# Performance work log

Hardware: AMD Instinct MI355X
Metric: run time of the kernel (lower is better)

## Reference

```python
import jax, jax.numpy as jnp
import numpy as np

DIM = 512
MAXP = 100
N_SAMPLED = MAXP - 2  # partitions 0 (whole) and 1 (singletons) handled analytically
KMAX = 6              # sampled partitions have 2..6 parts


def _make_part_masks(dim, n_sampled, kmax, seed=0):
    rng = np.random.default_rng(seed)
    masks = np.zeros((n_sampled, kmax, dim), dtype=bool)
    for p in range(n_sampled):
        n_parts = rng.integers(2, kmax + 1)
        assign = rng.integers(0, n_parts, size=dim)
        for k in range(n_parts):
            masks[p, k] = assign == k
    return masks


def setup_inputs() -> dict:
    key = jax.random.key(0)
    ks = jax.random.split(key, 10)
    B, S, D = 8, 4096, DIM
    x = jax.random.normal(ks[0], (B, S, D), dtype=jnp.float32)
    entropy_scales = jnp.ones((D,), dtype=jnp.float32)
    integration_weights = jnp.ones((MAXP,), dtype=jnp.float32)
    W1 = jax.random.normal(ks[1], (32, 1), dtype=jnp.float32) * 0.5
    b1 = jax.random.normal(ks[2], (32,), dtype=jnp.float32) * 0.1
    W2 = jax.random.normal(ks[3], (16, 32), dtype=jnp.float32) * 0.2
    b2 = jax.random.normal(ks[4], (16,), dtype=jnp.float32) * 0.1
    W3 = jax.random.normal(ks[5], (1, 16), dtype=jnp.float32) * 0.3
    b3 = jax.random.normal(ks[6], (1,), dtype=jnp.float32) * 0.1
    part_masks = jnp.asarray(_make_part_masks(D, N_SAMPLED, KMAX))  # [P,K,D] bool
    return {"x": x, "entropy_scales": entropy_scales,
            "integration_weights": integration_weights,
            "W1": W1, "b1": b1, "W2": W2, "b2": b2, "W3": W3, "b3": b3,
            "part_masks": part_masks}


def _phi(x, entropy_scales, integration_weights, W1, b1, W2, b2, W3, b3, part_masks):
    B, S, D = x.shape
    # ---- full-flatten entropy (per batch), H(softmax(x.reshape(B,-1))) ----
    lp = jax.nn.log_softmax(x.reshape(B, -1), axis=-1)
    H_full = -jnp.sum(jnp.exp(lp) * lp, axis=-1)                     # [B]
    h_full_scaled = H_full * entropy_scales.mean()                   # [B]
    h_whole = H_full.mean()                                          # partition idx 0

    # ---- singleton partition (idx 1): softmax over seq per (b,d) ----
    lps = jax.nn.log_softmax(x, axis=1)                              # [B,S,D]
    H_sd = -jnp.sum(jnp.exp(lps) * lps, axis=1)                      # [B,D]
    h_single = H_sd.mean(axis=0).sum()

    # ---- sampled partitions via masks: per part, softmax over (seq x part dims) ----
    xmax_d = x.max(axis=1)                                           # [B,D]
    ex = jnp.exp(x - xmax_d[:, None, :])                             # [B,S,D]
    e_d = ex.sum(axis=1)                                             # [B,D] sum exp(x - xmax_d)
    t_d = (ex * x).sum(axis=1)                                       # [B,D] sum exp(.)*x
    valid = part_masks.any(axis=-1)                                  # [P,K]
    neg = jnp.finfo(x.dtype).min
    gmax = jnp.max(jnp.where(part_masks[None], xmax_d[:, None, None, :], neg), axis=-1)  # [B,P,K]
    gmax = jnp.where(valid[None], gmax, 0.0)
    shift = jnp.exp(xmax_d[:, None, None, :] - gmax[..., None])      # [B,P,K,D] <= 1
    mf = part_masks.astype(x.dtype)
    Z = jnp.einsum('pkd,bd,bpkd->bpk', mf, e_d, shift)               # group partition fn
    T = jnp.einsum('pkd,bd,bpkd->bpk', mf, t_d, shift)
    Zs = jnp.where(valid[None], Z, 1.0)
    H_pk = gmax + jnp.log(Zs) - T / Zs                               # group entropy [B,P,K]
    H_pk = jnp.where(valid[None], H_pk, 0.0)
    h_sampled = H_pk.mean(axis=0).sum(axis=-1)                       # [P] sum of part entropies

    h_parts = jnp.concatenate([jnp.stack([h_whole, h_single]), h_sampled])   # [100]
    weighted = h_parts * jax.nn.sigmoid(integration_weights[: h_parts.shape[0]])
    min_part = weighted.min()

    raw_phi = h_full_scaled.mean() - min_part
    z = jnp.clip(raw_phi / 10.0, 0.0, 1.0)[None]                     # [1]
    h = jax.nn.relu(z @ W1.T + b1)
    h = jax.nn.relu(h @ W2.T + b2)
    conf = jax.nn.sigmoid(h @ W3.T + b3).squeeze(-1)                 # scalar
    return conf


def reference(x, entropy_scales, integration_weights, W1, b1, W2, b2, W3, b3, part_masks):
    return _phi(x, entropy_scales, integration_weights, W1, b1, W2, b2, W3, b3, part_masks)
```

## Files before the change

### kernel.cpp

```cpp
#include <hip/hip_runtime.h>
#include <math.h>

constexpr int Bv = 8;
constexpr int Sv = 4096;
constexpr int Dv = 512;
constexpr int NCv = 64;
constexpr int SCv = Sv / NCv;
constexpr int Pv = 98;
constexpr int Kv = 6;
constexpr int MAXPv = 100;

constexpr size_t OFF_MPART = 0;
constexpr size_t OFF_ZPART = OFF_MPART + (size_t)Bv * NCv * Dv;
constexpr size_t OFF_TPART = OFF_ZPART + (size_t)Bv * NCv * Dv;
constexpr size_t OFF_XMAX  = OFF_TPART + (size_t)Bv * NCv * Dv;
constexpr size_t OFF_ED    = OFF_XMAX + (size_t)Bv * Dv;
constexpr size_t OFF_TD    = OFF_ED   + (size_t)Bv * Dv;
constexpr size_t OFF_HFULL = OFF_TD   + (size_t)Bv * Dv;
constexpr size_t OFF_HSD   = OFF_HFULL + Bv;
constexpr size_t OFF_HBP   = OFF_HSD + Bv;
constexpr size_t OFF_ASSIGN = OFF_HBP + (size_t)Bv * Pv;

__device__ __forceinline__ float warpSum(float v) {
    for (int o = 32; o > 0; o >>= 1) v += __shfl_xor(v, o);
    return v;
}
__device__ __forceinline__ float warpMax(float v) {
    for (int o = 32; o > 0; o >>= 1) v = fmaxf(v, __shfl_xor(v, o));
    return v;
}
__device__ __forceinline__ float blockSum512(float v, float* red) {
    float s = warpSum(v);
    int lane = threadIdx.x & 63, w = threadIdx.x >> 6;
    __syncthreads();
    if (lane == 0) red[w] = s;
    __syncthreads();
    return red[0] + red[1] + red[2] + red[3] + red[4] + red[5] + red[6] + red[7];
}
__device__ __forceinline__ float blockMax512(float v, float* red) {
    float s = warpMax(v);
    int lane = threadIdx.x & 63, w = threadIdx.x >> 6;
    __syncthreads();
    if (lane == 0) red[w] = s;
    __syncthreads();
    float m = red[0];
    for (int i = 1; i < 8; i++) m = fmaxf(m, red[i]);
    return m;
}

__device__ __forceinline__ unsigned int encf(float f) {
    unsigned int u = __float_as_uint(f);
    return (u & 0x80000000u) ? ~u : (u | 0x80000000u);
}
__device__ __forceinline__ float decf(unsigned int u) {
    return (u & 0x80000000u) ? __uint_as_float(u ^ 0x80000000u) : __uint_as_float(~u);
}

#define UPD(v, m, z, t)                                        \
    {                                                          \
        float vv = (v);                                        \
        if (vv > m) {                                          \
            float r = __expf(m - vv);                          \
            z = z * r + 1.0f;                                  \
            t = t * r + vv;                                    \
            m = vv;                                            \
        } else {                                               \
            float e_ = __expf(vv - m);                         \
            z += e_;                                           \
            t += e_ * vv;                                      \
        }                                                      \
    }

__device__ __forceinline__ void mergeStats(float& m, float& z, float& t,
                                           float mb, float zb, float tb) {
    float nm = fmaxf(m, mb);
    float ra = __expf(m - nm);
    float rb = __expf(mb - nm);
    z = z * ra + zb * rb;
    t = t * ra + tb * rb;
    m = nm;
}

__global__ __launch_bounds__(512) void k_assign(const void* __restrict__ masks,
                                                float* __restrict__ ws) {
    int p = blockIdx.x;
    int d = threadIdx.x;
    __shared__ int f;
    if (d == 0) f = 0;
    __syncthreads();
    const unsigned int* mw = (const unsigned int*)masks;
    if (mw[d] > 1u || mw[d + 512] > 1u) atomicOr(&f, 1);
    __syncthreads();
    int is_u8 = f;

    unsigned char a = 255;
    if (is_u8) {
        const unsigned char* mb = (const unsigned char*)masks;
        for (int k = 0; k < Kv; k++) {
            if (mb[((size_t)p * Kv + k) * Dv + d]) { a = (unsigned char)k; break; }
        }
    } else {
        const int* mi = (const int*)masks;
        for (int k = 0; k < Kv; k++) {
            if (mi[((size_t)p * Kv + k) * Dv + d]) { a = (unsigned char)k; break; }
        }
    }
    ((unsigned char*)(ws + OFF_ASSIGN))[(size_t)p * Dv + d] = a;
}

__global__ __launch_bounds__(256) void k1_partial(const float* __restrict__ x,
                                                  float* __restrict__ ws) {
    int c = blockIdx.x;
    int b = blockIdx.y;
    int tid = threadIdx.x;
    int dg = tid & 127;
    int sl = tid >> 7;

    const float4* xv = (const float4*)x;
    float m0 = -INFINITY, m1 = -INFINITY, m2 = -INFINITY, m3 = -INFINITY;
    float z0 = 0.f, z1 = 0.f, z2 = 0.f, z3 = 0.f;
    float t0 = 0.f, t1 = 0.f, t2 = 0.f, t3 = 0.f;

    int sbase = c * SCv + sl;
    for (int i = 0; i < SCv / 2; i++) {
        int s = sbase + 2 * i;
        float4 v = xv[((size_t)b * Sv + s) * 128 + dg];
        UPD(v.x, m0, z0, t0);
        UPD(v.y, m1, z1, t1);
        UPD(v.z, m2, z2, t2);
        UPD(v.w, m3, z3, t3);
    }

    __shared__ float smm[128 * 4], smz[128 * 4], smt[128 * 4];
    if (sl == 1) {
        smm[dg * 4 + 0] = m0; smm[dg * 4 + 1] = m1; smm[dg * 4 + 2] = m2; smm[dg * 4 + 3] = m3;
        smz[dg * 4 + 0] = z0; smz[dg * 4 + 1] = z1; smz[dg * 4 + 2] = z2; smz[dg * 4 + 3] = z3;
        smt[dg * 4 + 0] = t0; smt[dg * 4 + 1] = t1; smt[dg * 4 + 2] = t2; smt[dg * 4 + 3] = t3;
    }
    __syncthreads();
    if (sl == 0) {
        mergeStats(m0, z0, t0, smm[dg * 4 + 0], smz[dg * 4 + 0], smt[dg * 4 + 0]);
        mergeStats(m1, z1, t1, smm[dg * 4 + 1], smz[dg * 4 + 1], smt[dg * 4 + 1]);
        mergeStats(m2, z2, t2, smm[dg * 4 + 2], smz[dg * 4 + 2], smt[dg * 4 + 2]);
        mergeStats(m3, z3, t3, smm[dg * 4 + 3], smz[dg * 4 + 3], smt[dg * 4 + 3]);

        size_t o = ((size_t)(b * NCv + c)) * 128 + dg;
        ((float4*)(ws + OFF_MPART))[o] = make_float4(m0, m1, m2, m3);
        ((float4*)(ws + OFF_ZPART))[o] = make_float4(z0, z1, z2, z3);
        ((float4*)(ws + OFF_TPART))[o] = make_float4(t0, t1, t2, t3);
    }
}

__global__ __launch_bounds__(512) void k2_combine(float* __restrict__ ws) {
    int b = blockIdx.x;
    int d = threadIdx.x;
    const float* mp = ws + OFF_MPART;
    const float* zp = ws + OFF_ZPART;
    const float* tp = ws + OFF_TPART;

    float m = -INFINITY, z = 0.f, t = 0.f;
    for (int c = 0; c < NCv; c++) {
        size_t idx = ((size_t)(b * NCv + c)) * Dv + d;
        mergeStats(m, z, t, mp[idx], zp[idx], tp[idx]);
    }

    ws[OFF_XMAX + (size_t)b * Dv + d] = m;
    ws[OFF_ED   + (size_t)b * Dv + d] = z;
    ws[OFF_TD   + (size_t)b * Dv + d] = t;

    float hsd = m + __logf(z) - t / z;

    __shared__ float red[8];
    float sum_h = blockSum512(hsd, red);
    float mb = blockMax512(m, red);
    float sc = __expf(m - mb);
    float zb = blockSum512(z * sc, red);
    float tb = blockSum512(t * sc, red);
    if (d == 0) {
        ws[OFF_HSD + b] = sum_h;
        ws[OFF_HFULL + b] = mb + __logf(zb) - tb / zb;
    }
}

__global__ __launch_bounds__(512) void k3_parts(float* __restrict__ ws) {
    int p = blockIdx.x;
    int b = blockIdx.y;
    int d = threadIdx.x;

    float xm = ws[OFF_XMAX + (size_t)b * Dv + d];
    float e  = ws[OFF_ED   + (size_t)b * Dv + d];
    float t  = ws[OFF_TD   + (size_t)b * Dv + d];
    int k = ((const unsigned char*)(ws + OFF_ASSIGN))[(size_t)p * Dv + d];

    __shared__ unsigned int gmu[Kv];
    __shared__ float sz[Kv], st[Kv], hk[Kv];
    const unsigned int ENC_NEGINF = 0x007FFFFFu;
    if (d < Kv) { gmu[d] = ENC_NEGINF; sz[d] = 0.f; st[d] = 0.f; }
    __syncthreads();
    if (k < Kv) atomicMax(&gmu[k], encf(xm));
    __syncthreads();
    if (k < Kv) {
        float g = decf(gmu[k]);
        float s = __expf(xm - g);
        atomicAdd(&sz[k], e * s);
        atomicAdd(&st[k], t * s);
    }
    __syncthreads();
    if (d < Kv) {
        float h = 0.f;
        unsigned int u = gmu[d];
        if (u != ENC_NEGINF) {
            float Z = sz[d];
            h = decf(u) + __logf(Z) - st[d] / Z;
        }
        hk[d] = h;
    }
    __syncthreads();
    if (d == 0)
        ws[OFF_HBP + (size_t)b * Pv + p] = hk[0] + hk[1] + hk[2] + hk[3] + hk[4] + hk[5];
}

__device__ __forceinline__ float sigmoidf(float v) { return 1.0f / (1.0f + __expf(-v)); }

__global__ __launch_bounds__(128) void k4_final(
    const float* __restrict__ es, const float* __restrict__ iw,
    const float* __restrict__ W1, const float* __restrict__ b1,
    const float* __restrict__ W2, const float* __restrict__ b2,
    const float* __restrict__ W3, const float* __restrict__ b3,
    const float* __restrict__ ws, float* __restrict__ out) {
    int tid = threadIdx.x;
    __shared__ float wgt[MAXPv];
    __shared__ float meanH_s;
    __shared__ float red[2];

    float v = es[tid] + es[tid + 128] + es[tid + 256] + es[tid + 384];
    float s64 = warpSum(v);
    int lane = tid & 63, w = tid >> 6;
    if (lane == 0) red[w] = s64;
    __syncthreads();
    float es_mean = (red[0] + red[1]) * (1.0f / 512.0f);

    if (tid < Pv) {
        float s = 0.f;
        for (int b = 0; b < Bv; b++) s += ws[OFF_HBP + (size_t)b * Pv + tid];
        wgt[tid + 2] = (s * (1.0f / Bv)) * sigmoidf(iw[tid + 2]);
    } else if (tid == Pv) {
        float s = 0.f;
        for (int b = 0; b < Bv; b++) s += ws[OFF_HFULL + b];
        float mh = s * (1.0f / Bv);
        meanH_s = mh;
        wgt[0] = mh * sigmoidf(iw[0]);
    } else if (tid == Pv + 1) {
        float s = 0.f;
        for (int b = 0; b < Bv; b++) s += ws[OFF_HSD + b];
        wgt[1] = (s * (1.0f / Bv)) * sigmoidf(iw[1]);
    }
    __syncthreads();

    if (tid == 0) {
        float mn = wgt[0];
        for (int i = 1; i < MAXPv; i++) mn = fminf(mn, wgt[i]);
        float raw = es_mean * meanH_s - mn;
        float z = fminf(fmaxf(raw * 0.1f, 0.0f), 1.0f);

        float h1[32];
        for (int j = 0; j < 32; j++) {
            float a = z * W1[j] + b1[j];
            h1[j] = a > 0.f ? a : 0.f;
        }
        float h2[16];
        for (int i = 0; i < 16; i++) {
            float a = b2[i];
            for (int j = 0; j < 32; j++) a += W2[i * 32 + j] * h1[j];
            h2[i] = a > 0.f ? a : 0.f;
        }
        float a = b3[0];
        for (int i = 0; i < 16; i++) a += W3[i] * h2[i];
        out[0] = sigmoidf(a);
    }
}

extern "C" void kernel_launch(void* const* d_in, const int* in_sizes, int n_in,
                              void* d_out, int out_size, void* d_ws, size_t ws_size,
                              hipStream_t stream) {
    const float* x  = (const float*)d_in[0];
    const float* es = (const float*)d_in[1];
    const float* iw = (const float*)d_in[2];
    const float* W1 = (const float*)d_in[3];
    const float* b1 = (const float*)d_in[4];
    const float* W2 = (const float*)d_in[5];
    const float* b2 = (const float*)d_in[6];
    const float* W3 = (const float*)d_in[7];
    const float* b3 = (const float*)d_in[8];
    const void* masks = d_in[9];
    float* ws = (float*)d_ws;
    float* out = (float*)d_out;

    k_assign<<<dim3(Pv), dim3(512), 0, stream>>>(masks, ws);
    k1_partial<<<dim3(NCv, Bv), dim3(256), 0, stream>>>(x, ws);
    k2_combine<<<dim3(Bv), dim3(512), 0, stream>>>(ws);
    k3_parts<<<dim3(Pv, Bv), dim3(512), 0, stream>>>(ws);
    k4_final<<<dim3(1), dim3(128), 0, stream>>>(es, iw, W1, b1, W2, b2, W3, b3, ws, out);
}
```

Baseline: 153.7 us.

## Fuse five kernels into two using last-block atomic counters

Cuts the pipeline from five launches to two. The per-batch combine now runs in the last-arriving block of the partial pass, found with an atomic counter, and the final scalar MLP runs in the last block of the partition pass. The mask-to-assignment decode moves into the partition kernel, and the shared-memory float atomics are replaced by per-k warp reductions. This removes launch and inter-kernel gaps, but adds a memset, threadfences, serial tail work in single blocks, and redundant mask decoding for every batch.

```diff
diff --git a/kernel.cpp b/kernel.cpp
--- a/kernel.cpp
+++ b/kernel.cpp
@@ -10,7 +10,7 @@
 constexpr int Kv = 6;
 constexpr int MAXPv = 100;
 
-constexpr size_t OFF_MPART = 0;
+constexpr size_t OFF_MPART = 16;
 constexpr size_t OFF_ZPART = OFF_MPART + (size_t)Bv * NCv * Dv;
 constexpr size_t OFF_TPART = OFF_ZPART + (size_t)Bv * NCv * Dv;
 constexpr size_t OFF_XMAX  = OFF_TPART + (size_t)Bv * NCv * Dv;
@@ -19,7 +19,6 @@
 constexpr size_t OFF_HFULL = OFF_TD   + (size_t)Bv * Dv;
 constexpr size_t OFF_HSD   = OFF_HFULL + Bv;
 constexpr size_t OFF_HBP   = OFF_HSD + Bv;
-constexpr size_t OFF_ASSIGN = OFF_HBP + (size_t)Bv * Pv;
 
 __device__ __forceinline__ float warpSum(float v) {
     for (int o = 32; o > 0; o >>= 1) v += __shfl_xor(v, o);
@@ -29,6 +28,22 @@
     for (int o = 32; o > 0; o >>= 1) v = fmaxf(v, __shfl_xor(v, o));
     return v;
 }
+__device__ __forceinline__ float blockSum256(float v, float* red) {
+    float s = warpSum(v);
+    int lane = threadIdx.x & 63, w = threadIdx.x >> 6;
+    __syncthreads();
+    if (lane == 0) red[w] = s;
+    __syncthreads();
+    return red[0] + red[1] + red[2] + red[3];
+}
+__device__ __forceinline__ float blockMax256(float v, float* red) {
+    float s = warpMax(v);
+    int lane = threadIdx.x & 63, w = threadIdx.x >> 6;
+    __syncthreads();
+    if (lane == 0) red[w] = s;
+    __syncthreads();
+    return fmaxf(fmaxf(red[0], red[1]), fmaxf(red[2], red[3]));
+}
 __device__ __forceinline__ float blockSum512(float v, float* red) {
     float s = warpSum(v);
     int lane = threadIdx.x & 63, w = threadIdx.x >> 6;
@@ -36,24 +51,6 @@
     if (lane == 0) red[w] = s;
     __syncthreads();
     return red[0] + red[1] + red[2] + red[3] + red[4] + red[5] + red[6] + red[7];
-}
-__device__ __forceinline__ float blockMax512(float v, float* red) {
-    float s = warpMax(v);
-    int lane = threadIdx.x & 63, w = threadIdx.x >> 6;
-    __syncthreads();
-    if (lane == 0) red[w] = s;
-    __syncthreads();
-    float m = red[0];
-    for (int i = 1; i < 8; i++) m = fmaxf(m, red[i]);
-    return m;
-}
-
-__device__ __forceinline__ unsigned int encf(float f) {
-    unsigned int u = __float_as_uint(f);
-    return (u & 0x80000000u) ? ~u : (u | 0x80000000u);
-}
-__device__ __forceinline__ float decf(unsigned int u) {
-    return (u & 0x80000000u) ? __uint_as_float(u ^ 0x80000000u) : __uint_as_float(~u);
 }
 
 #define UPD(v, m, z, t)                                        \
@@ -81,35 +78,11 @@
     m = nm;
 }
 
-__global__ __launch_bounds__(512) void k_assign(const void* __restrict__ masks,
-                                                float* __restrict__ ws) {
-    int p = blockIdx.x;
-    int d = threadIdx.x;
-    __shared__ int f;
-    if (d == 0) f = 0;
-    __syncthreads();
-    const unsigned int* mw = (const unsigned int*)masks;
-    if (mw[d] > 1u || mw[d + 512] > 1u) atomicOr(&f, 1);
-    __syncthreads();
-    int is_u8 = f;
-
-    unsigned char a = 255;
-    if (is_u8) {
-        const unsigned char* mb = (const unsigned char*)masks;
-        for (int k = 0; k < Kv; k++) {
-            if (mb[((size_t)p * Kv + k) * Dv + d]) { a = (unsigned char)k; break; }
-        }
-    } else {
-        const int* mi = (const int*)masks;
-        for (int k = 0; k < Kv; k++) {
-            if (mi[((size_t)p * Kv + k) * Dv + d]) { a = (unsigned char)k; break; }
-        }
-    }
-    ((unsigned char*)(ws + OFF_ASSIGN))[(size_t)p * Dv + d] = a;
-}
-
-__global__ __launch_bounds__(256) void k1_partial(const float* __restrict__ x,
-                                                  float* __restrict__ ws) {
+__device__ __forceinline__ float sigmoidf(float v) { return 1.0f / (1.0f + __expf(-v)); }
+
+__global__ __launch_bounds__(256) void k1_fused(const float* __restrict__ x,
+                                                float* __restrict__ ws,
+                                                int* __restrict__ ctr) {
     int c = blockIdx.x;
     int b = blockIdx.y;
     int tid = threadIdx.x;
@@ -131,7 +104,9 @@
         UPD(v.w, m3, z3, t3);
     }
 
-    __shared__ float smm[128 * 4], smz[128 * 4], smt[128 * 4];
+    __shared__ float smm[512], smz[512], smt[512];
+    __shared__ float red[4];
+    __shared__ int amLast;
     if (sl == 1) {
         smm[dg * 4 + 0] = m0; smm[dg * 4 + 1] = m1; smm[dg * 4 + 2] = m2; smm[dg * 4 + 3] = m3;
         smz[dg * 4 + 0] = z0; smz[dg * 4 + 1] = z1; smz[dg * 4 + 2] = z2; smz[dg * 4 + 3] = z3;
@@ -149,115 +124,152 @@
         ((float4*)(ws + OFF_ZPART))[o] = make_float4(z0, z1, z2, z3);
         ((float4*)(ws + OFF_TPART))[o] = make_float4(t0, t1, t2, t3);
     }
-}
-
-__global__ __launch_bounds__(512) void k2_combine(float* __restrict__ ws) {
-    int b = blockIdx.x;
-    int d = threadIdx.x;
+    __threadfence();
+    __syncthreads();
+    if (tid == 0) {
+        int old = atomicAdd(&ctr[b], 1);
+        amLast = (old == NCv - 1);
+    }
+    __syncthreads();
+    if (!amLast) return;
+    __threadfence();
+
     const float* mp = ws + OFF_MPART;
     const float* zp = ws + OFF_ZPART;
     const float* tp = ws + OFF_TPART;
-
-    float m = -INFINITY, z = 0.f, t = 0.f;
-    for (int c = 0; c < NCv; c++) {
-        size_t idx = ((size_t)(b * NCv + c)) * Dv + d;
-        mergeStats(m, z, t, mp[idx], zp[idx], tp[idx]);
-    }
-
-    ws[OFF_XMAX + (size_t)b * Dv + d] = m;
-    ws[OFF_ED   + (size_t)b * Dv + d] = z;
-    ws[OFF_TD   + (size_t)b * Dv + d] = t;
-
-    float hsd = m + __logf(z) - t / z;
-
-    __shared__ float red[8];
-    float sum_h = blockSum512(hsd, red);
-    float mb = blockMax512(m, red);
-    float sc = __expf(m - mb);
-    float zb = blockSum512(z * sc, red);
-    float tb = blockSum512(t * sc, red);
-    if (d == 0) {
-        ws[OFF_HSD + b] = sum_h;
+    float cm[2], cz[2], ct[2], ch[2];
+    for (int r = 0; r < 2; r++) {
+        int d = tid + 256 * r;
+        float m = -INFINITY, z = 0.f, t = 0.f;
+        for (int cc = 0; cc < NCv; cc++) {
+            size_t idx = ((size_t)(b * NCv + cc)) * Dv + d;
+            mergeStats(m, z, t, mp[idx], zp[idx], tp[idx]);
+        }
+        ws[OFF_XMAX + (size_t)b * Dv + d] = m;
+        ws[OFF_ED   + (size_t)b * Dv + d] = z;
+        ws[OFF_TD   + (size_t)b * Dv + d] = t;
+        cm[r] = m; cz[r] = z; ct[r] = t;
+        ch[r] = m + __logf(z) - t / z;
+    }
+    float hs = blockSum256(ch[0] + ch[1], red);
+    float mb = blockMax256(fmaxf(cm[0], cm[1]), red);
+    float s0 = __expf(cm[0] - mb), s1 = __expf(cm[1] - mb);
+    float zb = blockSum256(cz[0] * s0 + cz[1] * s1, red);
+    float tb = blockSum256(ct[0] * s0 + ct[1] * s1, red);
+    if (tid == 0) {
+        ws[OFF_HSD + b]   = hs;
         ws[OFF_HFULL + b] = mb + __logf(zb) - tb / zb;
     }
 }
 
-__global__ __launch_bounds__(512) void k3_parts(float* __restrict__ ws) {
-    int p = blockIdx.x;
-    int b = blockIdx.y;
-    int d = threadIdx.x;
-
-    float xm = ws[OFF_XMAX + (size_t)b * Dv + d];
-    float e  = ws[OFF_ED   + (size_t)b * Dv + d];
-    float t  = ws[OFF_TD   + (size_t)b * Dv + d];
-    int k = ((const unsigned char*)(ws + OFF_ASSIGN))[(size_t)p * Dv + d];
-
-    __shared__ unsigned int gmu[Kv];
-    __shared__ float sz[Kv], st[Kv], hk[Kv];
-    const unsigned int ENC_NEGINF = 0x007FFFFFu;
-    if (d < Kv) { gmu[d] = ENC_NEGINF; sz[d] = 0.f; st[d] = 0.f; }
-    __syncthreads();
-    if (k < Kv) atomicMax(&gmu[k], encf(xm));
-    __syncthreads();
-    if (k < Kv) {
-        float g = decf(gmu[k]);
-        float s = __expf(xm - g);
-        atomicAdd(&sz[k], e * s);
-        atomicAdd(&st[k], t * s);
-    }
-    __syncthreads();
-    if (d < Kv) {
-        float h = 0.f;
-        unsigned int u = gmu[d];
-        if (u != ENC_NEGINF) {
-            float Z = sz[d];
-            h = decf(u) + __logf(Z) - st[d] / Z;
-        }
-        hk[d] = h;
-    }
-    __syncthreads();
-    if (d == 0)
-        ws[OFF_HBP + (size_t)b * Pv + p] = hk[0] + hk[1] + hk[2] + hk[3] + hk[4] + hk[5];
-}
-
-__device__ __forceinline__ float sigmoidf(float v) { return 1.0f / (1.0f + __expf(-v)); }
-
-__global__ __launch_bounds__(128) void k4_final(
+__global__ __launch_bounds__(512) void k3_fused(
+    const void* __restrict__ masks,
     const float* __restrict__ es, const float* __restrict__ iw,
     const float* __restrict__ W1, const float* __restrict__ b1,
     const float* __restrict__ W2, const float* __restrict__ b2,
     const float* __restrict__ W3, const float* __restrict__ b3,
-    const float* __restrict__ ws, float* __restrict__ out) {
-    int tid = threadIdx.x;
+    float* __restrict__ ws, int* __restrict__ ctr,
+    float* __restrict__ out) {
+    int p = blockIdx.x;
+    int b = blockIdx.y;
+    int d = threadIdx.x;
+    int lane = d & 63, w = d >> 6;
+
+    __shared__ int f;
+    if (d == 0) f = 0;
+    __syncthreads();
+    const unsigned int* mwords = (const unsigned int*)masks;
+    if (mwords[d] > 1u) atomicOr(&f, 1);
+    __syncthreads();
+
+    int mk = 255;
+    if (f) {
+        const unsigned char* mbyt = (const unsigned char*)masks;
+        for (int k = 0; k < Kv; k++)
+            if (mbyt[((size_t)p * Kv + k) * Dv + d]) { mk = k; break; }
+    } else {
+        const int* mint = (const int*)masks;
+        for (int k = 0; k < Kv; k++)
+            if (mint[((size_t)p * Kv + k) * Dv + d]) { mk = k; break; }
+    }
+
+    float xm = ws[OFF_XMAX + (size_t)b * Dv + d];
+    float e  = ws[OFF_ED   + (size_t)b * Dv + d];
+    float t  = ws[OFF_TD   + (size_t)b * Dv + d];
+
+    __shared__ float lmax[8 * Kv], lz[8 * Kv], lt[8 * Kv];
+    __shared__ float gmax[Kv], hk[Kv];
+    __shared__ int amLast;
+
+    for (int k = 0; k < Kv; k++) {
+        float cv = (mk == k) ? xm : -INFINITY;
+        float wm = warpMax(cv);
+        if (lane == 0) lmax[w * Kv + k] = wm;
+    }
+    __syncthreads();
+    if (d < Kv) {
+        float g = lmax[d];
+        for (int ww = 1; ww < 8; ww++) g = fmaxf(g, lmax[ww * Kv + d]);
+        gmax[d] = g;
+    }
+    __syncthreads();
+
+    int mks = (mk < Kv) ? mk : 0;
+    float g = gmax[mks];
+    float s = __expf(xm - g);
+    float ez = e * s, tz = t * s;
+    for (int k = 0; k < Kv; k++) {
+        float cz = (mk == k) ? ez : 0.f;
+        float ctv = (mk == k) ? tz : 0.f;
+        float sz = warpSum(cz);
+        float st = warpSum(ctv);
+        if (lane == 0) { lz[w * Kv + k] = sz; lt[w * Kv + k] = st; }
+    }
+    __syncthreads();
+    if (d < Kv) {
+        float Z = 0.f, T = 0.f;
+        for (int ww = 0; ww < 8; ww++) { Z += lz[ww * Kv + d]; T += lt[ww * Kv + d]; }
+        float gm = gmax[d];
+        hk[d] = (gm > -INFINITY) ? gm + __logf(Z) - T / Z : 0.f;
+    }
+    __syncthreads();
+    if (d == 0)
+        ws[OFF_HBP + (size_t)b * Pv + p] = hk[0] + hk[1] + hk[2] + hk[3] + hk[4] + hk[5];
+
+    __threadfence();
+    __syncthreads();
+    if (d == 0) {
+        int old = atomicAdd(&ctr[8], 1);
+        amLast = (old == Pv * Bv - 1);
+    }
+    __syncthreads();
+    if (!amLast) return;
+    __threadfence();
+
     __shared__ float wgt[MAXPv];
     __shared__ float meanH_s;
-    __shared__ float red[2];
-
-    float v = es[tid] + es[tid + 128] + es[tid + 256] + es[tid + 384];
-    float s64 = warpSum(v);
-    int lane = tid & 63, w = tid >> 6;
-    if (lane == 0) red[w] = s64;
-    __syncthreads();
-    float es_mean = (red[0] + red[1]) * (1.0f / 512.0f);
-
-    if (tid < Pv) {
-        float s = 0.f;
-        for (int b = 0; b < Bv; b++) s += ws[OFF_HBP + (size_t)b * Pv + tid];
-        wgt[tid + 2] = (s * (1.0f / Bv)) * sigmoidf(iw[tid + 2]);
-    } else if (tid == Pv) {
-        float s = 0.f;
-        for (int b = 0; b < Bv; b++) s += ws[OFF_HFULL + b];
-        float mh = s * (1.0f / Bv);
+    __shared__ float red8[8];
+
+    float es_mean = blockSum512(es[d], red8) * (1.0f / Dv);
+
+    if (d < Pv) {
+        float sacc = 0.f;
+        for (int bb = 0; bb < Bv; bb++) sacc += ws[OFF_HBP + (size_t)bb * Pv + d];
+        wgt[d + 2] = (sacc * (1.0f / Bv)) * sigmoidf(iw[d + 2]);
+    } else if (d == Pv) {
+        float sacc = 0.f;
+        for (int bb = 0; bb < Bv; bb++) sacc += ws[OFF_HFULL + bb];
+        float mh = sacc * (1.0f / Bv);
         meanH_s = mh;
         wgt[0] = mh * sigmoidf(iw[0]);
-    } else if (tid == Pv + 1) {
-        float s = 0.f;
-        for (int b = 0; b < Bv; b++) s += ws[OFF_HSD + b];
-        wgt[1] = (s * (1.0f / Bv)) * sigmoidf(iw[1]);
-    }
-    __syncthreads();
-
-    if (tid == 0) {
+    } else if (d == Pv + 1) {
+        float sacc = 0.f;
+        for (int bb = 0; bb < Bv; bb++) sacc += ws[OFF_HSD + bb];
+        wgt[1] = (sacc * (1.0f / Bv)) * sigmoidf(iw[1]);
+    }
+    __syncthreads();
+
+    if (d == 0) {
         float mn = wgt[0];
         for (int i = 1; i < MAXPv; i++) mn = fminf(mn, wgt[i]);
         float raw = es_mean * meanH_s - mn;
@@ -294,11 +306,11 @@
     const float* b3 = (const float*)d_in[8];
     const void* masks = d_in[9];
     float* ws = (float*)d_ws;
+    int* ctr = (int*)d_ws;
     float* out = (float*)d_out;
 
-    k_assign<<<dim3(Pv), dim3(512), 0, stream>>>(masks, ws);
-    k1_partial<<<dim3(NCv, Bv), dim3(256), 0, stream>>>(x, ws);
-    k2_combine<<<dim3(Bv), dim3(512), 0, stream>>>(ws);
-    k3_parts<<<dim3(Pv, Bv), dim3(512), 0, stream>>>(ws);
-    k4_final<<<dim3(1), dim3(128), 0, stream>>>(es, iw, W1, b1, W2, b2, W3, b3, ws, out);
-}
+    hipMemsetAsync(d_ws, 0, 16 * sizeof(int), stream);
+    k1_fused<<<dim3(NCv, Bv), dim3(256), 0, stream>>>(x, ws, ctr);
+    k3_fused<<<dim3(Pv, Bv), dim3(512), 0, stream>>>(masks, es, iw, W1, b1, W2, b2,
+                                                     W3, b3, ws, ctr, out);
+}
```

Result: slower. 301.7 us (+96.2%).

## Fuse mask decoding into partition kernel and replace LDS atomics with warp reductions

Applied to the files above, without the earlier changes.

Removes the separate k_assign launch by having each k3_parts block decode its own partition assignment straight from the mask tensor. The shared-memory atomicMax/atomicAdd grouping is replaced by per-group wave-level max/sum shuffles plus a cross-wave combine in LDS. This drops one kernel launch and the atomic contention, but every batch block now re-reads the masks (8x redundant mask traffic). The dtype check also reads only the first 512 words instead of 1024.

```diff
diff --git a/kernel.cpp b/kernel.cpp
--- a/kernel.cpp
+++ b/kernel.cpp
@@ -19,7 +19,6 @@
 constexpr size_t OFF_HFULL = OFF_TD   + (size_t)Bv * Dv;
 constexpr size_t OFF_HSD   = OFF_HFULL + Bv;
 constexpr size_t OFF_HBP   = OFF_HSD + Bv;
-constexpr size_t OFF_ASSIGN = OFF_HBP + (size_t)Bv * Pv;
 
 __device__ __forceinline__ float warpSum(float v) {
     for (int o = 32; o > 0; o >>= 1) v += __shfl_xor(v, o);
@@ -46,14 +45,6 @@
     float m = red[0];
     for (int i = 1; i < 8; i++) m = fmaxf(m, red[i]);
     return m;
-}
-
-__device__ __forceinline__ unsigned int encf(float f) {
-    unsigned int u = __float_as_uint(f);
-    return (u & 0x80000000u) ? ~u : (u | 0x80000000u);
-}
-__device__ __forceinline__ float decf(unsigned int u) {
-    return (u & 0x80000000u) ? __uint_as_float(u ^ 0x80000000u) : __uint_as_float(~u);
 }
 
 #define UPD(v, m, z, t)                                        \
@@ -81,32 +72,7 @@
     m = nm;
 }
 
-__global__ __launch_bounds__(512) void k_assign(const void* __restrict__ masks,
-                                                float* __restrict__ ws) {
-    int p = blockIdx.x;
-    int d = threadIdx.x;
-    __shared__ int f;
-    if (d == 0) f = 0;
-    __syncthreads();
-    const unsigned int* mw = (const unsigned int*)masks;
-    if (mw[d] > 1u || mw[d + 512] > 1u) atomicOr(&f, 1);
-    __syncthreads();
-    int is_u8 = f;
-
-    unsigned char a = 255;
-    if (is_u8) {
-        const unsigned char* mb = (const unsigned char*)masks;
-        for (int k = 0; k < Kv; k++) {
-            if (mb[((size_t)p * Kv + k) * Dv + d]) { a = (unsigned char)k; break; }
-        }
-    } else {
-        const int* mi = (const int*)masks;
-        for (int k = 0; k < Kv; k++) {
-            if (mi[((size_t)p * Kv + k) * Dv + d]) { a = (unsigned char)k; break; }
-        }
-    }
-    ((unsigned char*)(ws + OFF_ASSIGN))[(size_t)p * Dv + d] = a;
-}
+__device__ __forceinline__ float sigmoidf(float v) { return 1.0f / (1.0f + __expf(-v)); }
 
 __global__ __launch_bounds__(256) void k1_partial(const float* __restrict__ x,
                                                   float* __restrict__ ws) {
@@ -131,7 +97,7 @@
         UPD(v.w, m3, z3, t3);
     }
 
-    __shared__ float smm[128 * 4], smz[128 * 4], smt[128 * 4];
+    __shared__ float smm[512], smz[512], smt[512];
     if (sl == 1) {
         smm[dg * 4 + 0] = m0; smm[dg * 4 + 1] = m1; smm[dg * 4 + 2] = m2; smm[dg * 4 + 3] = m3;
         smz[dg * 4 + 0] = z0; smz[dg * 4 + 1] = z1; smz[dg * 4 + 2] = z2; smz[dg * 4 + 3] = z3;
@@ -182,45 +148,73 @@
     }
 }
 
-__global__ __launch_bounds__(512) void k3_parts(float* __restrict__ ws) {
+__global__ __launch_bounds__(512) void k3_parts(const void* __restrict__ masks,
+                                                float* __restrict__ ws) {
     int p = blockIdx.x;
     int b = blockIdx.y;
     int d = threadIdx.x;
+    int lane = d & 63, w = d >> 6;
+
+    __shared__ int f;
+    if (d == 0) f = 0;
+    __syncthreads();
+    const unsigned int* mwords = (const unsigned int*)masks;
+    if (mwords[d] > 1u) f = 1;
+    __syncthreads();
+
+    int mk = 255;
+    if (f) {
+        const unsigned char* mbyt = (const unsigned char*)masks;
+        for (int k = 0; k < Kv; k++)
+            if (mbyt[((size_t)p * Kv + k) * Dv + d]) { mk = k; break; }
+    } else {
+        const int* mint = (const int*)masks;
+        for (int k = 0; k < Kv; k++)
+            if (mint[((size_t)p * Kv + k) * Dv + d]) { mk = k; break; }
+    }
 
     float xm = ws[OFF_XMAX + (size_t)b * Dv + d];
     float e  = ws[OFF_ED   + (size_t)b * Dv + d];
     float t  = ws[OFF_TD   + (size_t)b * Dv + d];
-    int k = ((const unsigned char*)(ws + OFF_ASSIGN))[(size_t)p * Dv + d];
-
-    __shared__ unsigned int gmu[Kv];
-    __shared__ float sz[Kv], st[Kv], hk[Kv];
-    const unsigned int ENC_NEGINF = 0x007FFFFFu;
-    if (d < Kv) { gmu[d] = ENC_NEGINF; sz[d] = 0.f; st[d] = 0.f; }
-    __syncthreads();
-    if (k < Kv) atomicMax(&gmu[k], encf(xm));
-    __syncthreads();
-    if (k < Kv) {
-        float g = decf(gmu[k]);
-        float s = __expf(xm - g);
-        atomicAdd(&sz[k], e * s);
-        atomicAdd(&st[k], t * s);
+
+    __shared__ float lmax[8 * Kv], lz[8 * Kv], lt[8 * Kv];
+    __shared__ float gmax[Kv], hk[Kv];
+
+    for (int k = 0; k < Kv; k++) {
+        float cv = (mk == k) ? xm : -INFINITY;
+        float wm = warpMax(cv);
+        if (lane == 0) lmax[w * Kv + k] = wm;
     }
     __syncthreads();
     if (d < Kv) {
-        float h = 0.f;
-        unsigned int u = gmu[d];
-        if (u != ENC_NEGINF) {
-            float Z = sz[d];
-            h = decf(u) + __logf(Z) - st[d] / Z;
-        }
-        hk[d] = h;
+        float g = lmax[d];
+        for (int ww = 1; ww < 8; ww++) g = fmaxf(g, lmax[ww * Kv + d]);
+        gmax[d] = g;
+    }
+    __syncthreads();
+
+    int mks = (mk < Kv) ? mk : 0;
+    float g = gmax[mks];
+    float s = __expf(xm - g);
+    float ez = e * s, tz = t * s;
+    for (int k = 0; k < Kv; k++) {
+        float cz = (mk == k) ? ez : 0.f;
+        float ctv = (mk == k) ? tz : 0.f;
+        float sz = warpSum(cz);
+        float st = warpSum(ctv);
+        if (lane == 0) { lz[w * Kv + k] = sz; lt[w * Kv + k] = st; }
+    }
+    __syncthreads();
+    if (d < Kv) {
+        float Z = 0.f, T = 0.f;
+        for (int ww = 0; ww < 8; ww++) { Z += lz[ww * Kv + d]; T += lt[ww * Kv + d]; }
+        float gm = gmax[d];
+        hk[d] = (gm > -INFINITY) ? gm + __logf(Z) - T / Z : 0.f;
     }
     __syncthreads();
     if (d == 0)
         ws[OFF_HBP + (size_t)b * Pv + p] = hk[0] + hk[1] + hk[2] + hk[3] + hk[4] + hk[5];
 }
-
-__device__ __forceinline__ float sigmoidf(float v) { return 1.0f / (1.0f + __expf(-v)); }
 
 __global__ __launch_bounds__(128) void k4_final(
     const float* __restrict__ es, const float* __restrict__ iw,
@@ -296,9 +290,8 @@
     float* ws = (float*)d_ws;
     float* out = (float*)d_out;
 
-    k_assign<<<dim3(Pv), dim3(512), 0, stream>>>(masks, ws);
     k1_partial<<<dim3(NCv, Bv), dim3(256), 0, stream>>>(x, ws);
     k2_combine<<<dim3(Bv), dim3(512), 0, stream>>>(ws);
-    k3_parts<<<dim3(Pv, Bv), dim3(512), 0, stream>>>(ws);
+    k3_parts<<<dim3(Pv, Bv), dim3(512), 0, stream>>>(masks, ws);
     k4_final<<<dim3(1), dim3(128), 0, stream>>>(es, iw, W1, b1, W2, b2, W3, b3, ws, out);
 }
```

Result: no change. 155.6 us (+1.2%).
